# Performance work log

Hardware: AMD Instinct MI355X
Metric: run time of the kernel (lower is better)

## Reference

```python
import jax, jax.numpy as jnp
import numpy as np

jax.config.update("jax_enable_x64", True)

TOL = 1e-06


def setup_inputs() -> dict:
    key = jax.random.key(0)
    k1, k2 = jax.random.split(key)
    n, d = 4096, 128
    output = jax.random.normal(k1, (n, d), dtype=jnp.float32)
    # target: square roots of patristic distances -> nonnegative
    target = jax.random.uniform(k2, (n, n), dtype=jnp.float32) * 2.0
    return {"output": output, "target": target}


def reference(output, target):
    # Torch module casts to double before all math
    out = output.astype(jnp.float64)
    tgt = target.astype(jnp.float64)
    n = out.shape[0]

    # Lorentz inner product: B = outer(s, s) - out @ out.T, s = sqrt(1 + ||o||^2)
    s = jnp.sqrt(1.0 + jnp.sum(out * out, axis=1))          # [n]
    B = s[:, None] * s[None, :] - out @ out.T               # [n, n]

    # Clamp near-1 entries exactly to 1 (torch: B[(B-1).abs() < tol] = 1.0)
    clamp = jnp.abs(B - 1.0) < TOL
    # Safe acosh: evaluate at 2.0 where clamped to avoid inf/nan, then set dist=0 there
    B_safe = jnp.where(clamp, 2.0, B)
    dist = jnp.where(clamp, 0.0, jnp.arccosh(B_safe))       # acosh(1) == 0

    # Strictly-lower-triangular masked MAE
    tril_mask = jnp.tril(jnp.ones((n, n), dtype=jnp.float64), k=-1)
    loss = jnp.sum(jnp.abs(dist - tgt) * tril_mask) / (n * (n - 1))
    return loss
```

## Files before the change

kernel.cpp:

```cpp
#include <hip/hip_runtime.h>
#include <math.h>

#define N 4096
#define D 128
#define TS 64
#define NT (N / TS)
#define NBLK (NT * (NT + 1) / 2)

typedef __attribute__((ext_vector_type(8))) short short8;
typedef __attribute__((ext_vector_type(4))) float f32x4;

__global__ __launch_bounds__(256)
void prep_kernel(const float* __restrict__ O,
                 unsigned int* __restrict__ Obf_packed,
                 float* __restrict__ s) {
    const int wave = threadIdx.x >> 6;
    const int lane = threadIdx.x & 63;
    const int row  = blockIdx.x * 4 + wave;
    const float2 v = *(const float2*)(O + (size_t)row * D + 2 * lane);
    const unsigned int ux = __float_as_uint(v.x);
    const unsigned int uy = __float_as_uint(v.y);
    const unsigned int bx = (ux + 0x7FFFu + ((ux >> 16) & 1u)) >> 16;
    const unsigned int by = (uy + 0x7FFFu + ((uy >> 16) & 1u)) >> 16;
    Obf_packed[row * (D / 2) + lane] = bx | (by << 16);
    float acc = v.x * v.x + v.y * v.y;
    #pragma unroll
    for (int off = 32; off > 0; off >>= 1)
        acc += __shfl_down(acc, off, 64);
    if (lane == 0) s[row] = sqrtf(1.0f + acc);
}

__device__ __forceinline__ float acosh_dist(float B) {
    if (fabsf(B - 1.0f) < 1e-6f) return 0.0f;
    const float Bc = fmaxf(B, 1.0f);
    return logf(Bc + sqrtf(fmaf(Bc, Bc, -1.0f)));
}

__global__ __launch_bounds__(256, 4)
void tile_loss_kernel(const unsigned short* __restrict__ Obf,
                      const float* __restrict__ s,
                      const float* __restrict__ tgt,
                      float* __restrict__ partials) {
    __shared__ float wsum[4];

    const int t = blockIdx.x;
    int ti = (int)((sqrtf(8.0f * (float)t + 1.0f) - 1.0f) * 0.5f);
    while ((ti + 1) * (ti + 2) / 2 <= t) ti++;
    while (ti * (ti + 1) / 2 > t) ti--;
    const int tj = t - ti * (ti + 1) / 2;

    const int tid  = threadIdx.x;
    const int wave = tid >> 6;
    const int lane = tid & 63;
    const int quad = lane >> 4;
    const int l16  = lane & 15;

    const int ib = ti * TS + wave * 16;
    const int jb = tj * TS;

    f32x4 acc[4] = {};

    #pragma unroll
    for (int kk = 0; kk < 4; kk++) {
        const int kof = kk * 32 + quad * 8;
        const short8 a = *(const short8*)(Obf + (size_t)(ib + l16) * D + kof);
        short8 b[4];
        #pragma unroll
        for (int n = 0; n < 4; n++)
            b[n] = *(const short8*)(Obf + (size_t)(jb + n * 16 + l16) * D + kof);
        #pragma unroll
        for (int n = 0; n < 4; n++)
            acc[n] = __builtin_amdgcn_mfma_f32_16x16x32_bf16(a, b[n], acc[n], 0, 0, 0);
    }

    float sj[4];
    #pragma unroll
    for (int n = 0; n < 4; n++) sj[n] = s[jb + n * 16 + l16];

    const int i0 = ib + quad * 4;
    float si[4], tv[4][4];
    #pragma unroll
    for (int r = 0; r < 4; r++) {
        si[r] = s[i0 + r];
        const float* trow = tgt + (size_t)(i0 + r) * N + jb;
        #pragma unroll
        for (int n = 0; n < 4; n++)
            tv[r][n] = trow[n * 16 + l16];
    }

    float lsum = 0.0f;
    if (ti != tj) {
        #pragma unroll
        for (int r = 0; r < 4; r++)
            #pragma unroll
            for (int n = 0; n < 4; n++) {
                const float B = fmaf(si[r], sj[n], -acc[n][r]);
                lsum += fabsf(acosh_dist(B) - tv[r][n]);
            }
    } else {
        #pragma unroll
        for (int r = 0; r < 4; r++) {
            const int i = i0 + r;
            #pragma unroll
            for (int n = 0; n < 4; n++) {
                const int j = jb + n * 16 + l16;
                if (j < i) {
                    const float B = fmaf(si[r], sj[n], -acc[n][r]);
                    lsum += fabsf(acosh_dist(B) - tv[r][n]);
                }
            }
        }
    }

    #pragma unroll
    for (int off = 32; off > 0; off >>= 1)
        lsum += __shfl_down(lsum, off, 64);
    if (lane == 0) wsum[wave] = lsum;
    __syncthreads();
    if (tid == 0)
        partials[t] = wsum[0] + wsum[1] + wsum[2] + wsum[3];
}

__global__ __launch_bounds__(256)
void final_reduce_kernel(const float* __restrict__ partials,
                         float* __restrict__ loss) {
    __shared__ float wsum[4];
    const int tid  = threadIdx.x;
    const int wave = tid >> 6;
    const int lane = tid & 63;
    float acc = 0.0f;
    for (int i = tid; i < NBLK; i += 256) acc += partials[i];
    #pragma unroll
    for (int off = 32; off > 0; off >>= 1)
        acc += __shfl_down(acc, off, 64);
    if (lane == 0) wsum[wave] = acc;
    __syncthreads();
    if (tid == 0) {
        const float tot = wsum[0] + wsum[1] + wsum[2] + wsum[3];
        loss[0] = tot * (1.0f / ((float)N * (float)(N - 1)));
    }
}

extern "C" void kernel_launch(void* const* d_in, const int* in_sizes, int n_in,
                              void* d_out, int out_size, void* d_ws, size_t ws_size,
                              hipStream_t stream) {
    const float* O   = (const float*)d_in[0];
    const float* tgt = (const float*)d_in[1];
    float* loss = (float*)d_out;

    unsigned int* Obf_packed = (unsigned int*)d_ws;
    unsigned short* Obf      = (unsigned short*)d_ws;
    float* s        = (float*)((char*)d_ws + (size_t)N * D * 2);
    float* partials = s + N;

    prep_kernel<<<N / 4, 256, 0, stream>>>(O, Obf_packed, s);
    tile_loss_kernel<<<NBLK, 256, 0, stream>>>(Obf, s, tgt, partials);
    final_reduce_kernel<<<1, 256, 0, stream>>>(partials, loss);
}
```

Before: 115.4 us.

## Stage target tile via coalesced float4 loads into LDS, batch operand loads

The target tile is now read with 16-byte float4 loads into a padded shared-memory tile, issued before the MFMA loop, instead of scattered 4-byte per-lane reads issued after it. Operand loads for pairs of k-steps are batched to expose more memory-level parallelism. logf is replaced by the fast __log2f intrinsic times ln2. This adds an LDS buffer and a block barrier, which may reduce occupancy, and the fast log is slightly less accurate.

```diff
diff --git a/kernel.cpp b/kernel.cpp
--- a/kernel.cpp
+++ b/kernel.cpp
@@ -6,6 +6,7 @@
 #define TS 64
 #define NT (N / TS)
 #define NBLK (NT * (NT + 1) / 2)
+#define TPAD 68
 
 typedef __attribute__((ext_vector_type(8))) short short8;
 typedef __attribute__((ext_vector_type(4))) float f32x4;
@@ -33,7 +34,7 @@
 __device__ __forceinline__ float acosh_dist(float B) {
     if (fabsf(B - 1.0f) < 1e-6f) return 0.0f;
     const float Bc = fmaxf(B, 1.0f);
-    return logf(Bc + sqrtf(fmaf(Bc, Bc, -1.0f)));
+    return __log2f(Bc + sqrtf(fmaf(Bc, Bc, -1.0f))) * 0.6931471805599453f;
 }
 
 __global__ __launch_bounds__(256, 4)
@@ -41,6 +42,7 @@
                       const float* __restrict__ s,
                       const float* __restrict__ tgt,
                       float* __restrict__ partials) {
+    __shared__ float T[TS][TPAD];
     __shared__ float wsum[4];
 
     const int t = blockIdx.x;
@@ -55,38 +57,53 @@
     const int quad = lane >> 4;
     const int l16  = lane & 15;
 
-    const int ib = ti * TS + wave * 16;
-    const int jb = tj * TS;
+    const int ib0 = ti * TS;
+    const int jb  = tj * TS;
+    const int ib  = ib0 + wave * 16;
 
-    f32x4 acc[4] = {};
-
-    #pragma unroll
-    for (int kk = 0; kk < 4; kk++) {
-        const int kof = kk * 32 + quad * 8;
-        const short8 a = *(const short8*)(Obf + (size_t)(ib + l16) * D + kof);
-        short8 b[4];
+    {
+        const int r = tid >> 4;
+        const int c = (tid & 15) * 4;
+        float4 tg[4];
         #pragma unroll
-        for (int n = 0; n < 4; n++)
-            b[n] = *(const short8*)(Obf + (size_t)(jb + n * 16 + l16) * D + kof);
+        for (int p = 0; p < 4; p++)
+            tg[p] = *(const float4*)(tgt + (size_t)(ib0 + p * 16 + r) * N + jb + c);
         #pragma unroll
-        for (int n = 0; n < 4; n++)
-            acc[n] = __builtin_amdgcn_mfma_f32_16x16x32_bf16(a, b[n], acc[n], 0, 0, 0);
+        for (int p = 0; p < 4; p++)
+            *(float4*)&T[p * 16 + r][c] = tg[p];
     }
 
     float sj[4];
     #pragma unroll
     for (int n = 0; n < 4; n++) sj[n] = s[jb + n * 16 + l16];
+    const int r0 = wave * 16 + quad * 4;
+    float si[4];
+    #pragma unroll
+    for (int r = 0; r < 4; r++) si[r] = s[ib0 + r0 + r];
 
-    const int i0 = ib + quad * 4;
-    float si[4], tv[4][4];
+    f32x4 acc[4] = {};
+    const unsigned short* arow = Obf + (size_t)(ib + l16) * D + quad * 8;
     #pragma unroll
-    for (int r = 0; r < 4; r++) {
-        si[r] = s[i0 + r];
-        const float* trow = tgt + (size_t)(i0 + r) * N + jb;
+    for (int kp = 0; kp < 2; kp++) {
+        const int kof = kp * 64;
+        const short8 a0 = *(const short8*)(arow + kof);
+        const short8 a1 = *(const short8*)(arow + kof + 32);
+        short8 b0[4], b1[4];
+        #pragma unroll
+        for (int n = 0; n < 4; n++) {
+            const unsigned short* brow = Obf + (size_t)(jb + n * 16 + l16) * D + quad * 8;
+            b0[n] = *(const short8*)(brow + kof);
+            b1[n] = *(const short8*)(brow + kof + 32);
+        }
         #pragma unroll
         for (int n = 0; n < 4; n++)
-            tv[r][n] = trow[n * 16 + l16];
+            acc[n] = __builtin_amdgcn_mfma_f32_16x16x32_bf16(a0, b0[n], acc[n], 0, 0, 0);
+        #pragma unroll
+        for (int n = 0; n < 4; n++)
+            acc[n] = __builtin_amdgcn_mfma_f32_16x16x32_bf16(a1, b1[n], acc[n], 0, 0, 0);
     }
+
+    __syncthreads();
 
     float lsum = 0.0f;
     if (ti != tj) {
@@ -94,19 +111,21 @@
         for (int r = 0; r < 4; r++)
             #pragma unroll
             for (int n = 0; n < 4; n++) {
-                const float B = fmaf(si[r], sj[n], -acc[n][r]);
-                lsum += fabsf(acosh_dist(B) - tv[r][n]);
+                const float B  = fmaf(si[r], sj[n], -acc[n][r]);
+                const float tv = T[r0 + r][n * 16 + l16];
+                lsum += fabsf(acosh_dist(B) - tv);
             }
     } else {
         #pragma unroll
         for (int r = 0; r < 4; r++) {
-            const int i = i0 + r;
+            const int i = ib0 + r0 + r;
             #pragma unroll
             for (int n = 0; n < 4; n++) {
                 const int j = jb + n * 16 + l16;
                 if (j < i) {
-                    const float B = fmaf(si[r], sj[n], -acc[n][r]);
-                    lsum += fabsf(acosh_dist(B) - tv[r][n]);
+                    const float B  = fmaf(si[r], sj[n], -acc[n][r]);
+                    const float tv = T[r0 + r][n * 16 + l16];
+                    lsum += fabsf(acosh_dist(B) - tv);
                 }
             }
         }
```

New measurement: 114.5 us. About the same (-0.8%).
